# Optimization experiments

Measured on AMD Instinct MI355X. Metric: run time of the kernel, lower is better.

The kernel has to match this reference:

```python
import jax, jax.numpy as jnp
import numpy as np

C = 256
NUM_HEADS = 4
NBLK = 6  # 3 stages x depth 2
WS = (2, 8, 8)   # 3D window
SS = (1, 4, 4)   # shift for odd blocks
N_WIN = WS[0] * WS[1] * WS[2]  # 128 tokens per window
RPB_SIZE = (2 * WS[0] - 1) * (2 * WS[1] - 1) * (2 * WS[2] - 1)  # 675


def _rel_index():
    coords = np.stack(np.meshgrid(np.arange(WS[0]), np.arange(WS[1]), np.arange(WS[2]), indexing='ij'))
    coords = coords.reshape(3, -1)
    rel = (coords[:, :, None] - coords[:, None, :]).transpose(1, 2, 0)
    rel[:, :, 0] += WS[0] - 1
    rel[:, :, 1] += WS[1] - 1
    rel[:, :, 2] += WS[2] - 1
    rel[:, :, 0] *= (2 * WS[1] - 1) * (2 * WS[2] - 1)
    rel[:, :, 1] *= (2 * WS[2] - 1)
    return jnp.asarray(rel.sum(-1))  # [N_WIN, N_WIN]

REL_IDX = _rel_index()


def window_partition(x):
    # [B,D,H,W,C] -> [B*nW, N_WIN, C]
    B, D, H, W, Cc = x.shape
    x = x.reshape(B, D // WS[0], WS[0], H // WS[1], WS[1], W // WS[2], WS[2], Cc)
    return x.transpose(0, 1, 3, 5, 2, 4, 6, 7).reshape(-1, N_WIN, Cc)


def window_reverse(win, B, D, H, W):
    Cc = win.shape[-1]
    x = win.reshape(B, D // WS[0], H // WS[1], W // WS[2], WS[0], WS[1], WS[2], Cc)
    return x.transpose(0, 1, 4, 2, 5, 3, 6, 7).reshape(B, D, H, W, Cc)


def attn_mask(D, H, W):
    # standard shifted-window mask, computed on host constants
    img = np.zeros((1, D, H, W, 1), np.float32)
    cnt = 0
    for d in (slice(0, -WS[0]), slice(-WS[0], -SS[0]), slice(-SS[0], None)):
        for h in (slice(0, -WS[1]), slice(-WS[1], -SS[1]), slice(-SS[1], None)):
            for w in (slice(0, -WS[2]), slice(-WS[2], -SS[2]), slice(-SS[2], None)):
                img[:, d, h, w, :] = cnt
                cnt += 1
    mw = img.reshape(1, D // WS[0], WS[0], H // WS[1], WS[1], W // WS[2], WS[2], 1)
    mw = mw.transpose(0, 1, 3, 5, 2, 4, 6, 7).reshape(-1, N_WIN)
    diff = mw[:, None, :] - mw[:, :, None]
    return jnp.asarray(np.where(diff != 0, -100.0, 0.0).astype(np.float32))  # [nW,N,N]


def layer_norm(x, g, b):
    mu = x.mean(-1, keepdims=True)
    var = ((x - mu) ** 2).mean(-1, keepdims=True)
    return (x - mu) * jax.lax.rsqrt(var + 1e-5) * g + b


def setup_inputs() -> dict:
    key = jax.random.key(0)
    ks = jax.random.split(key, 10)
    f = jax.random.normal
    s = 0.02
    return dict(
        x=f(ks[0], (2, 2, 2, 4096, C), jnp.float32),
        n1w=jnp.ones((NBLK, C), jnp.float32), n1b=jnp.zeros((NBLK, C), jnp.float32),
        qkv_w=f(ks[1], (NBLK, C, 3 * C), jnp.float32) * s, qkv_b=jnp.zeros((NBLK, 3 * C), jnp.float32),
        rpb=f(ks[2], (NBLK, RPB_SIZE, NUM_HEADS), jnp.float32) * s,
        proj_w=f(ks[3], (NBLK, C, C), jnp.float32) * s, proj_b=jnp.zeros((NBLK, C), jnp.float32),
        n2w=jnp.ones((NBLK, C), jnp.float32), n2b=jnp.zeros((NBLK, C), jnp.float32),
        mlp1_w=f(ks[4], (NBLK, C, 4 * C), jnp.float32) * s, mlp1_b=jnp.zeros((NBLK, 4 * C), jnp.float32),
        mlp2_w=f(ks[5], (NBLK, 4 * C, C), jnp.float32) * s, mlp2_b=jnp.zeros((NBLK, C), jnp.float32),
        exp_v_w=f(ks[6], (C, 2 * C), jnp.float32) * s,
        exp_v_nw=jnp.ones((C,), jnp.float32), exp_v_nb=jnp.zeros((C,), jnp.float32),
        exp_t_w=f(ks[7], (C, 2 * C), jnp.float32) * s,
        exp_t_nw=jnp.ones((C,), jnp.float32), exp_t_nb=jnp.zeros((C,), jnp.float32),
    )


def reference(x, n1w, n1b, qkv_w, qkv_b, rpb, proj_w, proj_b, n2w, n2b,
              mlp1_w, mlp1_b, mlp2_w, mlp2_b,
              exp_v_w, exp_v_nw, exp_v_nb, exp_t_w, exp_t_nw, exp_t_nb):
    B, T, V, L, _ = x.shape
    H = W = int(round(np.sqrt(L)))
    NH = NUM_HEADS
    dh = C // NH

    def block(h, i, D, shifted, mask):
        # h: [B, D, L, C]
        sc = h
        y = layer_norm(h, n1w[i], n1b[i]).reshape(B, D, H, W, C)
        if shifted:
            y = jnp.roll(y, (-SS[0], -SS[1], -SS[2]), axis=(1, 2, 3))
        win = window_partition(y)  # [B*nW, N, C]
        qkv = (win @ qkv_w[i] + qkv_b[i]).reshape(-1, N_WIN, 3, NH, dh)
        q, k, v = jnp.moveaxis(qkv, 2, 0)              # [B*nW, N, NH, dh]
        q = q.transpose(0, 2, 1, 3)
        k = k.transpose(0, 2, 1, 3)
        v = v.transpose(0, 2, 1, 3)                     # [B*nW, NH, N, dh]
        attn = jnp.einsum('whqd,whkd->whqk', q, k) * (dh ** -0.5)
        attn = attn + rpb[i][REL_IDX].transpose(2, 0, 1)[None]
        if mask is not None:
            nW = mask.shape[0]
            attn = attn.reshape(B, nW, NH, N_WIN, N_WIN) + mask[None, :, None]
            attn = attn.reshape(-1, NH, N_WIN, N_WIN)
        attn = jax.nn.softmax(attn, axis=-1)
        out = jnp.einsum('whqk,whkd->whqd', attn, v).transpose(0, 2, 1, 3).reshape(-1, N_WIN, C)
        out = out @ proj_w[i] + proj_b[i]
        y = window_reverse(out, B, D, H, W)
        if shifted:
            y = jnp.roll(y, (SS[0], SS[1], SS[2]), axis=(1, 2, 3))
        h = sc + y.reshape(B, D, L, C)
        z = layer_norm(h, n2w[i], n2b[i])
        z = jax.nn.gelu(z @ mlp1_w[i] + mlp1_b[i], approximate=False) @ mlp2_w[i] + mlp2_b[i]
        return h + z

    def stage(h, i0, D):
        mask = attn_mask(D, H, W)
        h = block(h, i0, D, False, None)
        h = block(h, i0 + 1, D, True, mask)
        return h

    # stage 1: swin over D = T*V
    h = x.reshape(B, T * V, L, C)
    h = stage(h, 0, T * V)
    h = h.reshape(B, T, V, L, C)

    # stage 2: view patch expand (V -> 2V) + swin
    h = (h @ exp_v_w).reshape(B, T, V, L, 2, C).transpose(0, 1, 2, 4, 3, 5).reshape(B, T, 2 * V, L, C)
    h = layer_norm(h, exp_v_nw, exp_v_nb)
    V2 = 2 * V
    h = h.reshape(B, T * V2, L, C)
    h = stage(h, 2, T * V2)
    h = h.reshape(B, T, V2, L, C)

    # stage 3: temporal patch expand (T -> 2T) + swin
    h = (h @ exp_t_w).reshape(B, T, V2, L, 2, C).transpose(0, 1, 4, 2, 3, 5).reshape(B, 2 * T, V2, L, C)
    h = layer_norm(h, exp_t_nw, exp_t_nb)
    T2 = 2 * T
    h = h.reshape(B, T2 * V2, L, C)
    h = stage(h, 4, T2 * V2)
    return h.reshape(B, T2, V2, L, C)
```

## Files before the change

kernel.cpp:

```cpp
#include <hip/hip_runtime.h>

typedef __bf16 bf16x8 __attribute__((ext_vector_type(8)));
typedef float f32x4 __attribute__((ext_vector_type(4)));
typedef unsigned short u16;
typedef unsigned int u32;

__device__ __forceinline__ u16 f2b(float f) {
    union { float f; u32 u; } v; v.f = f;
    u32 r = v.u + 0x7fffu + ((v.u >> 16) & 1u);
    return (u16)(r >> 16);
}
__device__ __forceinline__ float b2f(u16 u) {
    union { u32 u; float f; } v; v.u = ((u32)u) << 16; return v.f;
}
__device__ __forceinline__ void gl_lds16(const u16* g, u16* l) {
    __builtin_amdgcn_global_load_lds(
        (const __attribute__((address_space(1))) void*)g,
        (__attribute__((address_space(3))) void*)l, 16, 0, 0);
}

__global__ __launch_bounds__(256) void ln_kernel(
    const float* __restrict__ h, u16* __restrict__ out,
    const float* __restrict__ g, const float* __restrict__ bb,
    int D, int dsh, int shifted, int mode)
{
    const int lane = threadIdx.x & 63;
    const int t = blockIdx.x * 4 + (threadIdx.x >> 6);
    const float4 xv = *(const float4*)(h + (size_t)t * 256 + lane * 4);
    float s = xv.x + xv.y + xv.z + xv.w;
    float s2 = xv.x*xv.x + xv.y*xv.y + xv.z*xv.z + xv.w*xv.w;
    #pragma unroll
    for (int o = 32; o > 0; o >>= 1) { s += __shfl_xor(s, o); s2 += __shfl_xor(s2, o); }
    const float mu = s * 0.00390625f;
    const float var = s2 * 0.00390625f - mu * mu;
    const float rs = 1.0f / sqrtf(var + 1e-5f);
    const int c0 = lane * 4;
    const float4 gv = *(const float4*)(g + c0);
    const float4 bv = *(const float4*)(bb + c0);
    ushort4 o4;
    o4.x = f2b((xv.x - mu) * rs * gv.x + bv.x);
    o4.y = f2b((xv.y - mu) * rs * gv.y + bv.y);
    o4.z = f2b((xv.z - mu) * rs * gv.z + bv.z);
    o4.w = f2b((xv.w - mu) * rs * gv.w + bv.w);
    size_t oidx;
    if (mode == 1) {
        oidx = (size_t)t * 256 + c0;
    } else {
        const int b = t >> (dsh + 12);
        const int rem = t & ((1 << (dsh + 12)) - 1);
        int d = rem >> 12;
        const int l = rem & 4095;
        int hh = l >> 6, ww = l & 63;
        if (shifted) { d = d ? d - 1 : D - 1; hh = (hh - 4) & 63; ww = (ww - 4) & 63; }
        const int widx = (b << (dsh + 5)) + ((d >> 1) << 6) + ((hh >> 3) << 3) + (ww >> 3);
        const int n = ((d & 1) << 6) + ((hh & 7) << 3) + (ww & 7);
        oidx = ((size_t)(widx * 128 + n)) * 256 + c0;
    }
    *(ushort4*)(out + oidx) = o4;
}

__global__ __launch_bounds__(256) void cast_kernel(const float* __restrict__ in, u16* __restrict__ out, int n4)
{
    const int i = blockIdx.x * 256 + threadIdx.x;
    if (i >= n4) return;
    const float4 v = ((const float4*)in)[i];
    ushort4 o; o.x = f2b(v.x); o.y = f2b(v.y); o.z = f2b(v.z); o.w = f2b(v.w);
    ((ushort4*)out)[i] = o;
}

__global__ __launch_bounds__(256) void wt_kernel(const float* __restrict__ src, u16* __restrict__ dst, int K, int N)
{
    const size_t base = (size_t)blockIdx.y * K * N;
    const int idx = blockIdx.x * 256 + threadIdx.x;
    const int k = idx / N, n = idx - k * N;
    dst[base + (size_t)n * K + k] = f2b(src[base + idx]);
}

struct GemmP {
    const u16* A; const u16* Bt;
    int K;
    const float* bias;
    u16* outb;
    float* outf;
    const float* hin; float* hout;
    int D, shifted, nwsh, row_off;
};

template <int EPI>
__global__ __launch_bounds__(256, 2) void gemm_kernel(GemmP p)
{
    __shared__ __align__(16) char smem[33792];
    float* CF = (float*)smem;

    const int tid = threadIdx.x;
    const int m0 = blockIdx.x * 128, n0 = blockIdx.y * 128;
    const int K = p.K;
    const int lane = tid & 63;
    const int wv = tid >> 6;
    const int wm = (wv & 1) * 64, wn = (wv >> 1) * 64;
    const int l16 = lane & 15, quad = lane >> 4;

    f32x4 acc[4][4];
    #pragma unroll
    for (int a = 0; a < 4; a++)
        #pragma unroll
        for (int b = 0; b < 4; b++)
            acc[a][b] = f32x4{0.f, 0.f, 0.f, 0.f};

    const int lrow = lane >> 2;
    const int c16s = (lane & 3) ^ (lrow & 3);
    const int rA0 = wv * 16;
    const u16* Ag = p.A + (size_t)(m0 + rA0 + lrow) * K + c16s * 8;
    const u16* Bg = p.Bt + (size_t)(n0 + rA0 + lrow) * K + c16s * 8;
    const size_t j64 = (size_t)64 * K;
    const int fslot = (quad ^ (l16 & 3)) * 8;

    {
        u16* Al = (u16*)smem + rA0 * 32;
        u16* Bl = (u16*)(smem + 8192) + rA0 * 32;
        gl_lds16(Ag, Al);
        gl_lds16(Ag + j64, Al + 64 * 32);
        gl_lds16(Bg, Bl);
        gl_lds16(Bg + j64, Bl + 64 * 32);
    }
    __syncthreads();

    int kb = 0;
    for (int k0 = 0; k0 < K; k0 += 32, kb ^= 1) {
        if (k0 + 32 < K) {
            char* nb = smem + (kb ^ 1) * 16384;
            u16* Al = (u16*)nb + rA0 * 32;
            u16* Bl = (u16*)(nb + 8192) + rA0 * 32;
            gl_lds16(Ag + k0 + 32, Al);
            gl_lds16(Ag + j64 + k0 + 32, Al + 64 * 32);
            gl_lds16(Bg + k0 + 32, Bl);
            gl_lds16(Bg + j64 + k0 + 32, Bl + 64 * 32);
        }
        const u16* As = (const u16*)(smem + kb * 16384);
        const u16* Bs = (const u16*)(smem + kb * 16384 + 8192);
        bf16x8 af[4], bfr[4];
        #pragma unroll
        for (int mt = 0; mt < 4; mt++) af[mt] = *(const bf16x8*)(As + (wm + mt * 16 + l16) * 32 + fslot);
        #pragma unroll
        for (int nt = 0; nt < 4; nt++) bfr[nt] = *(const bf16x8*)(Bs + (wn + nt * 16 + l16) * 32 + fslot);
        #pragma unroll
        for (int mt = 0; mt < 4; mt++)
            #pragma unroll
            for (int nt = 0; nt < 4; nt++)
                acc[mt][nt] = __builtin_amdgcn_mfma_f32_16x16x32_bf16(af[mt], bfr[nt], acc[mt][nt], 0, 0, 0);
        __syncthreads();
    }

    const int crow = tid >> 2;
    const int p4 = (tid & 3) * 4;
    #pragma unroll
    for (int c = 0; c < 2; c++) {
        if (c) __syncthreads();
        if ((wv & 1) == c) {
            #pragma unroll
            for (int mt = 0; mt < 4; mt++)
                #pragma unroll
                for (int nt = 0; nt < 4; nt++)
                    #pragma unroll
                    for (int i = 0; i < 4; i++)
                        CF[(mt * 16 + quad * 4 + i) * 132 + wn + nt * 16 + l16] = acc[mt][nt][i];
        }
        __syncthreads();
        const int rowg = m0 + c * 64 + crow;
        size_t tokbase = 0;
        if constexpr (EPI == 1) {
            const int widx = rowg >> 7, n = rowg & 127;
            const int b = widx >> p.nwsh, rem = widx & ((1 << p.nwsh) - 1);
            int dd = ((rem >> 6) << 1) + (n >> 6);
            int hh = (((rem >> 3) & 7) << 3) + ((n >> 3) & 7);
            int ww = ((rem & 7) << 3) + (n & 7);
            if (p.shifted) { dd = (dd + 1 == p.D) ? 0 : dd + 1; hh = (hh + 4) & 63; ww = (ww + 4) & 63; }
            tokbase = ((size_t)((b * p.D + dd) * 4096 + hh * 64 + ww)) * 256;
        } else if constexpr (EPI == 3) {
            tokbase = (size_t)(p.row_off + rowg) * 256;
        }
        #pragma unroll
        for (int j = 0; j < 8; j++) {
            const int colf = j * 16 + p4;
            const int colg = n0 + colf;
            const float4 t = *(const float4*)(CF + crow * 132 + colf);
            const float4 bi = (EPI <= 3) ? *(const float4*)(p.bias + colg) : float4{0.f,0.f,0.f,0.f};
            if constexpr (EPI == 0) {
                const float sc = (colg < 256) ? 0.125f : 1.0f;
                ushort4 pk;
                pk.x = f2b((t.x + bi.x) * sc);
                pk.y = f2b((t.y + bi.y) * sc);
                pk.z = f2b((t.z + bi.z) * sc);
                pk.w = f2b((t.w + bi.w) * sc);
                *(ushort4*)(p.outb + (size_t)rowg * 768 + colg) = pk;
            } else if constexpr (EPI == 1 || EPI == 3) {
                const float* hi = p.hin + tokbase + colg;
                float* ho = p.hout + tokbase + colg;
                const float4 r = *(const float4*)hi;
                float4 o;
                o.x = r.x + t.x + bi.x;
                o.y = r.y + t.y + bi.y;
                o.z = r.z + t.z + bi.z;
                o.w = r.w + t.w + bi.w;
                *(float4*)ho = o;
            } else if constexpr (EPI == 2) {
                float4 g4;
                g4.x = t.x + bi.x; g4.y = t.y + bi.y; g4.z = t.z + bi.z; g4.w = t.w + bi.w;
                ushort4 pk;
                pk.x = f2b(0.5f * g4.x * (1.0f + erff(g4.x * 0.7071067811865475f)));
                pk.y = f2b(0.5f * g4.y * (1.0f + erff(g4.y * 0.7071067811865475f)));
                pk.z = f2b(0.5f * g4.z * (1.0f + erff(g4.z * 0.7071067811865475f)));
                pk.w = f2b(0.5f * g4.w * (1.0f + erff(g4.w * 0.7071067811865475f)));
                *(ushort4*)(p.outb + (size_t)rowg * 1024 + colg) = pk;
            } else {
                *(float4*)(p.outf + (size_t)rowg * 512 + colg) = t;
            }
        }
    }
}

struct MlpP {
    const u16* A;
    const u16* W1t;
    const u16* W2t;
    const float* b1;
    const float* b2;
    const float* hin;
    float* hout;
};

__global__ __launch_bounds__(512, 1) void mlp_fused_kernel(MlpP p)
{
    __shared__ __align__(16) char smem[149504];
    u16* S = (u16*)(smem + 131072);
    float* CF = (float*)smem;

    const int tid = threadIdx.x;
    const int lane = tid & 63;
    const int wv = tid >> 6;
    const int l16 = lane & 15, quad = lane >> 4;
    const int tok0 = blockIdx.x * 128;

    const int wm = (wv & 3) * 32;
    const int wn1 = (wv >> 2) * 32;
    const int wn2 = (wv >> 2) * 128;
    const int fslot = (quad ^ (l16 & 3)) * 8;

    const int srow = lane >> 2;
    const int sslotg = (lane & 3) ^ (srow & 3);
    const int w1row = (wv & 3) * 16 + srow;

    bf16x8 afr[2][8];
    #pragma unroll
    for (int mt = 0; mt < 2; mt++)
        #pragma unroll
        for (int kt = 0; kt < 8; kt++)
            afr[mt][kt] = *(const bf16x8*)(p.A + (size_t)(tok0 + wm + mt * 16 + l16) * 256 + kt * 32 + quad * 8);

    f32x4 acc2[2][8];
    #pragma unroll
    for (int mt = 0; mt < 2; mt++)
        #pragma unroll
        for (int nt = 0; nt < 8; nt++)
            acc2[mt][nt] = f32x4{0.f, 0.f, 0.f, 0.f};

    float b2v[8];
    #pragma unroll
    for (int nt = 0; nt < 8; nt++) b2v[nt] = p.b2[wn2 + nt * 16 + l16];

    auto stage = [&](int c) {
        char* w1b = smem + (c & 1) * 32768;
        char* w2b = smem + 65536 + (c & 1) * 32768;
        #pragma unroll
        for (int pp = 0; pp < 4; pp++) {
            const int panel = pp * 2 + (wv >> 2);
            gl_lds16(p.W1t + (size_t)(c * 64 + w1row) * 256 + panel * 32 + sslotg * 8,
                     (u16*)(w1b + pp * 8192 + wv * 1024));
        }
        #pragma unroll
        for (int pp = 0; pp < 4; pp++) {
            const int row = (pp & 1) * 128 + wv * 16 + srow;
            const int panel = pp >> 1;
            gl_lds16(p.W2t + (size_t)row * 1024 + c * 64 + panel * 32 + sslotg * 8,
                     (u16*)(w2b + pp * 8192 + wv * 1024));
        }
    };

    stage(0);
    __syncthreads();

    for (int c = 0; c < 16; c++) {
        if (c + 1 < 16) stage(c + 1);

        const u16* W1c = (const u16*)(smem + (c & 1) * 32768);
        f32x4 acc1[2][2];
        #pragma unroll
        for (int mt = 0; mt < 2; mt++)
            #pragma unroll
            for (int nt = 0; nt < 2; nt++)
                acc1[mt][nt] = f32x4{0.f, 0.f, 0.f, 0.f};
        #pragma unroll
        for (int kt = 0; kt < 8; kt++) {
            bf16x8 bw[2];
            #pragma unroll
            for (int nt = 0; nt < 2; nt++)
                bw[nt] = *(const bf16x8*)(W1c + kt * 2048 + (wn1 + nt * 16 + l16) * 32 + fslot);
            #pragma unroll
            for (int mt = 0; mt < 2; mt++)
                #pragma unroll
                for (int nt = 0; nt < 2; nt++)
                    acc1[mt][nt] = __builtin_amdgcn_mfma_f32_16x16x32_bf16(afr[mt][kt], bw[nt], acc1[mt][nt], 0, 0, 0);
        }

        #pragma unroll
        for (int nt = 0; nt < 2; nt++) {
            const float b1v = p.b1[c * 64 + wn1 + nt * 16 + l16];
            #pragma unroll
            for (int mt = 0; mt < 2; mt++)
                #pragma unroll
                for (int i = 0; i < 4; i++) {
                    const float x = acc1[mt][nt][i] + b1v;
                    const float g = 0.5f * x * (1.0f + erff(x * 0.7071067811865475f));
                    S[(wm + mt * 16 + quad * 4 + i) * 72 + wn1 + nt * 16 + l16] = f2b(g);
                }
        }
        __syncthreads();

        const u16* W2c = (const u16*)(smem + 65536 + (c & 1) * 32768);
        #pragma unroll
        for (int kt = 0; kt < 2; kt++) {
            bf16x8 ap[2], bw[8];
            #pragma unroll
            for (int mt = 0; mt < 2; mt++)
                ap[mt] = *(const bf16x8*)(S + (wm + mt * 16 + l16) * 72 + kt * 32 + quad * 8);
            #pragma unroll
            for (int nt = 0; nt < 8; nt++)
                bw[nt] = *(const bf16x8*)(W2c + kt * 8192 + (wn2 + nt * 16 + l16) * 32 + fslot);
            #pragma unroll
            for (int mt = 0; mt < 2; mt++)
                #pragma unroll
                for (int nt = 0; nt < 8; nt++)
                    acc2[mt][nt] = __builtin_amdgcn_mfma_f32_16x16x32_bf16(ap[mt], bw[nt], acc2[mt][nt], 0, 0, 0);
        }
        __syncthreads();
    }

    #pragma unroll
    for (int cc = 0; cc < 2; cc++) {
        __syncthreads();
        if (((wv & 3) >> 1) == cc) {
            const int rb = wm & 63;
            #pragma unroll
            for (int mt = 0; mt < 2; mt++)
                #pragma unroll
                for (int nt = 0; nt < 8; nt++)
                    #pragma unroll
                    for (int i = 0; i < 4; i++)
                        CF[(rb + mt * 16 + quad * 4 + i) * 260 + wn2 + nt * 16 + l16] = acc2[mt][nt][i] + b2v[nt];
        }
        __syncthreads();
        #pragma unroll
        for (int jj = 0; jj < 8; jj++) {
            const int idx = jj * 512 + tid;
            const int row = idx >> 6, c4 = (idx & 63) << 2;
            const size_t g = (size_t)(tok0 + cc * 64 + row) * 256 + c4;
            const float4 t = *(const float4*)(CF + row * 260 + c4);
            const float4 r = *(const float4*)(p.hin + g);
            float4 o;
            o.x = t.x + r.x; o.y = t.y + r.y; o.z = t.z + r.z; o.w = t.w + r.w;
            *(float4*)(p.hout + g) = o;
        }
    }
}

__global__ __launch_bounds__(256, 2) void attn_mfma_kernel(
    const u16* __restrict__ qkv, u16* __restrict__ att,
    const float* __restrict__ rpbp, int D, int shifted, int w0g, int nwsh)
{
    __shared__ __align__(16) char smem[57856];
    u16* Qs = (u16*)smem;
    u16* Ks = (u16*)(smem + 18432);
    u16* Ps = (u16*)smem;
    u16* Vt = (u16*)(smem + 36864);
    float* rb = (float*)(smem + 54272);
    int* lbl = (int*)(smem + 56972);

    const int wloc = blockIdx.x;
    const int head = blockIdx.y;
    const int tid = threadIdx.x;
    const u16* base = qkv + (size_t)wloc * 98304;

    #pragma unroll
    for (int it = 0; it < 4; it++) {
        const int id = it * 256 + tid;
        const int row = id >> 3, oct = id & 7;
        const size_t ro = (size_t)row * 768 + head * 64 + oct * 8;
        *(uint4*)(Qs + row * 72 + oct * 8) = *(const uint4*)(base + ro);
        *(uint4*)(Ks + row * 72 + oct * 8) = *(const uint4*)(base + ro + 256);
        uint4 vv = *(const uint4*)(base + ro + 512);
        const u16* vp = (const u16*)&vv;
        #pragma unroll
        for (int q = 0; q < 8; q++) Vt[(oct * 8 + q) * 136 + row] = vp[q];
    }
    for (int j = tid; j < 675; j += 256) rb[j] = rpbp[j * 4 + head];
    if (tid < 128) {
        int lv = 0;
        if (shifted) {
            const int widx = w0g + wloc;
            const int rem = widx & ((1 << nwsh) - 1);
            const int d0 = rem >> 6, h0 = (rem >> 3) & 7, w0 = rem & 7;
            const int wd = tid >> 6, wh = (tid >> 3) & 7, ww = tid & 7;
            const int rd = (d0 < (D >> 1) - 1) ? 0 : (1 + wd);
            const int rh = (h0 < 7) ? 0 : (1 + (wh >= 4));
            const int rw = (w0 < 7) ? 0 : (1 + (ww >= 4));
            lv = rd * 9 + rh * 3 + rw;
        }
        lbl[tid] = lv;
    }
    __syncthreads();

    const int wq = tid >> 6;
    const int lane = tid & 63;
    const int l16 = lane & 15, quad = lane >> 4;
    const int myrow0 = wq * 32;

    f32x4 sc[2][8];
    #pragma unroll
    for (int mt = 0; mt < 2; mt++)
        #pragma unroll
        for (int nt = 0; nt < 8; nt++)
            sc[mt][nt] = f32x4{0.f, 0.f, 0.f, 0.f};
    #pragma unroll
    for (int kt = 0; kt < 2; kt++) {
        bf16x8 aq[2];
        #pragma unroll
        for (int mt = 0; mt < 2; mt++)
            aq[mt] = *(const bf16x8*)(Qs + (myrow0 + mt * 16 + l16) * 72 + kt * 32 + quad * 8);
        bf16x8 bk[8];
        #pragma unroll
        for (int nt = 0; nt < 8; nt++)
            bk[nt] = *(const bf16x8*)(Ks + (nt * 16 + l16) * 72 + kt * 32 + quad * 8);
        #pragma unroll
        for (int mt = 0; mt < 2; mt++)
            #pragma unroll
            for (int nt = 0; nt < 8; nt++)
                sc[mt][nt] = __builtin_amdgcn_mfma_f32_16x16x32_bf16(aq[mt], bk[nt], sc[mt][nt], 0, 0, 0);
    }

    float linv[2][4];
    #pragma unroll
    for (int mt = 0; mt < 2; mt++) {
        #pragma unroll
        for (int i = 0; i < 4; i++) {
            const int row = myrow0 + mt * 16 + quad * 4 + i;
            const int rbase = ((row >> 6) + 1) * 225 + (((row >> 3) & 7) + 7) * 15 + ((row & 7) + 7);
            const int lq = lbl[row];
            float mx = -1e30f;
            float sv[8];
            #pragma unroll
            for (int nt = 0; nt < 8; nt++) {
                const int col = nt * 16 + l16;
                float v = sc[mt][nt][i] + rb[rbase - (col >> 6) * 225 - ((col >> 3) & 7) * 15 - (col & 7)];
                if (shifted && lq != lbl[col]) v -= 100.0f;
                sv[nt] = v;
                mx = fmaxf(mx, v);
            }
            #pragma unroll
            for (int o = 1; o < 16; o <<= 1) mx = fmaxf(mx, __shfl_xor(mx, o));
            float l = 0.0f;
            #pragma unroll
            for (int nt = 0; nt < 8; nt++) {
                const float pp = __expf(sv[nt] - mx);
                sc[mt][nt][i] = pp;
                l += pp;
            }
            #pragma unroll
            for (int o = 1; o < 16; o <<= 1) l += __shfl_xor(l, o);
            linv[mt][i] = 1.0f / l;
        }
    }

    __syncthreads();
    #pragma unroll
    for (int mt = 0; mt < 2; mt++)
        #pragma unroll
        for (int nt = 0; nt < 8; nt++)
            #pragma unroll
            for (int i = 0; i < 4; i++)
                Ps[(myrow0 + mt * 16 + quad * 4 + i) * 136 + nt * 16 + l16] = f2b(sc[mt][nt][i]);

    f32x4 oc[2][4];
    #pragma unroll
    for (int mt = 0; mt < 2; mt++)
        #pragma unroll
        for (int nt = 0; nt < 4; nt++)
            oc[mt][nt] = f32x4{0.f, 0.f, 0.f, 0.f};
    #pragma unroll
    for (int kt = 0; kt < 4; kt++) {
        bf16x8 ap[2];
        #pragma unroll
        for (int mt = 0; mt < 2; mt++)
            ap[mt] = *(const bf16x8*)(Ps + (myrow0 + mt * 16 + l16) * 136 + kt * 32 + quad * 8);
        bf16x8 bv[4];
        #pragma unroll
        for (int nt = 0; nt < 4; nt++)
            bv[nt] = *(const bf16x8*)(Vt + (nt * 16 + l16) * 136 + kt * 32 + quad * 8);
        #pragma unroll
        for (int mt = 0; mt < 2; mt++)
            #pragma unroll
            for (int nt = 0; nt < 4; nt++)
                oc[mt][nt] = __builtin_amdgcn_mfma_f32_16x16x32_bf16(ap[mt], bv[nt], oc[mt][nt], 0, 0, 0);
    }

    #pragma unroll
    for (int mt = 0; mt < 2; mt++)
        #pragma unroll
        for (int nt = 0; nt < 4; nt++)
            #pragma unroll
            for (int i = 0; i < 4; i++) {
                const int row = myrow0 + mt * 16 + quad * 4 + i;
                const int col = nt * 16 + l16;
                att[(size_t)(wloc * 128 + row) * 256 + head * 64 + col] = f2b(oc[mt][nt][i] * linv[mt][i]);
            }
}

__global__ __launch_bounds__(256) void expand_ln_kernel(
    const float* __restrict__ sc, float* __restrict__ hout,
    const float* __restrict__ g, const float* __restrict__ bb,
    int it0, int typ)
{
    const int lane = threadIdx.x & 63;
    const int ot = blockIdx.x * 4 + (threadIdx.x >> 6);
    const int itl = ot >> 1, e = ot & 1;
    const float4 xv = *(const float4*)(sc + (size_t)itl * 512 + e * 256 + lane * 4);
    float s = xv.x + xv.y + xv.z + xv.w;
    float s2 = xv.x*xv.x + xv.y*xv.y + xv.z*xv.z + xv.w*xv.w;
    #pragma unroll
    for (int o = 32; o > 0; o >>= 1) { s += __shfl_xor(s, o); s2 += __shfl_xor(s2, o); }
    const float mu = s * 0.00390625f;
    const float var = s2 * 0.00390625f - mu * mu;
    const float rs = 1.0f / sqrtf(var + 1e-5f);
    const int c0 = lane * 4;
    const float4 gv = *(const float4*)(g + c0);
    const float4 bv = *(const float4*)(bb + c0);
    float4 y;
    y.x = (xv.x - mu) * rs * gv.x + bv.x;
    y.y = (xv.y - mu) * rs * gv.y + bv.y;
    y.z = (xv.z - mu) * rs * gv.z + bv.z;
    y.w = (xv.w - mu) * rs * gv.w + bv.w;
    const int it = it0 + itl;
    size_t otg;
    if (typ == 0) {
        const int b = it >> 14, rr = it & 16383;
        const int t = rr >> 13, v = (rr >> 12) & 1, l = rr & 4095;
        otg = (size_t)(((b * 2 + t) * 4 + v * 2 + e) * 4096 + l);
    } else {
        const int b = it >> 15, rr = it & 32767;
        const int t = rr >> 14, v2 = (rr >> 12) & 3, l = rr & 4095;
        otg = (size_t)(((b * 4 + t * 2 + e) * 4 + v2) * 4096 + l);
    }
    *(float4*)(hout + otg * 256 + c0) = y;
}

extern "C" void kernel_launch(void* const* d_in, const int* in_sizes, int n_in,
                              void* d_out, int out_size, void* d_ws, size_t ws_size,
                              hipStream_t stream)
{
    const float* x      = (const float*)d_in[0];
    const float* n1w    = (const float*)d_in[1];
    const float* n1b    = (const float*)d_in[2];
    const float* qkv_w  = (const float*)d_in[3];
    const float* qkv_b  = (const float*)d_in[4];
    const float* rpb    = (const float*)d_in[5];
    const float* proj_w = (const float*)d_in[6];
    const float* proj_b = (const float*)d_in[7];
    const float* n2w    = (const float*)d_in[8];
    const float* n2b    = (const float*)d_in[9];
    const float* mlp1_w = (const float*)d_in[10];
    const float* mlp1_b = (const float*)d_in[11];
    const float* mlp2_w = (const float*)d_in[12];
    const float* mlp2_b = (const float*)d_in[13];
    const float* expv_w = (const float*)d_in[14];
    const float* expv_nw= (const float*)d_in[15];
    const float* expv_nb= (const float*)d_in[16];
    const float* expt_w = (const float*)d_in[17];
    const float* expt_nw= (const float*)d_in[18];
    const float* expt_nb= (const float*)d_in[19];
    (void)in_sizes; (void)n_in; (void)out_size;

    if (ws_size < 352321536ULL) return;

    char* ws = (char*)d_ws;
    float* h    = (float*)ws;
    u16*  winb  = (u16*)(ws + 134217728LL);
    u16*  att   = (u16*)(ws + 134217728LL + 67108864LL);
    char* scr   = ws + 134217728LL + 2LL * 67108864LL;
    u16*  scrb  = (u16*)scr;
    float* scrf = (float*)scr;
    u16* qkvT   = (u16*)(ws + 134217728LL + 3LL * 67108864LL);
    u16* projT  = qkvT + 6 * 768 * 256;
    u16* mlp1T  = projT + 6 * 256 * 256;
    u16* mlp2T  = mlp1T + 6 * 1024 * 256;
    u16* expvT  = mlp2T + 6 * 256 * 1024;
    u16* exptT  = expvT + 512 * 256;

    wt_kernel<<<dim3(768, 6), 256, 0, stream>>>(qkv_w, qkvT, 256, 768);
    wt_kernel<<<dim3(256, 6), 256, 0, stream>>>(proj_w, projT, 256, 256);
    wt_kernel<<<dim3(1024, 6), 256, 0, stream>>>(mlp1_w, mlp1T, 256, 1024);
    wt_kernel<<<dim3(1024, 6), 256, 0, stream>>>(mlp2_w, mlp2T, 1024, 256);
    wt_kernel<<<dim3(512, 1), 256, 0, stream>>>(expv_w, expvT, 256, 512);
    wt_kernel<<<dim3(512, 1), 256, 0, stream>>>(expt_w, exptT, 256, 512);
    hipMemcpyAsync(h, x, 33554432ULL, hipMemcpyDeviceToDevice, stream);

    for (int s = 0; s < 3; s++) {
        const int D = 4 << s;
        const int dsh = 2 + s;
        const int nwsh = dsh + 5;
        const int tokens = 2 * D * 4096;
        const int nch = tokens / 32768;
        for (int j = 0; j < 2; j++) {
            const int i = 2 * s + j;
            ln_kernel<<<dim3(tokens / 4), 256, 0, stream>>>(h, winb, n1w + i * 256, n1b + i * 256, D, dsh, j, 0);
            for (int c = 0; c < nch; c++) {
                GemmP gq{};
                gq.A = winb + (size_t)c * 32768 * 256;
                gq.Bt = qkvT + (size_t)i * 768 * 256;
                gq.K = 256; gq.bias = qkv_b + i * 768; gq.outb = scrb;
                gemm_kernel<0><<<dim3(256, 6), 256, 0, stream>>>(gq);
                attn_mfma_kernel<<<dim3(256, 4), 256, 0, stream>>>(scrb, att + (size_t)c * 32768 * 256,
                                                                   rpb + i * 675 * 4, D, j, c * 256, nwsh);
            }
            GemmP gp{};
            gp.A = att; gp.Bt = projT + (size_t)i * 256 * 256; gp.K = 256;
            gp.bias = proj_b + i * 256; gp.hin = h; gp.hout = h;
            gp.D = D; gp.shifted = j; gp.nwsh = nwsh;
            gemm_kernel<1><<<dim3(tokens / 128, 2), 256, 0, stream>>>(gp);
            ln_kernel<<<dim3(tokens / 4), 256, 0, stream>>>(h, winb, n2w + i * 256, n2b + i * 256, D, dsh, 0, 1);
            MlpP mp{};
            mp.A = winb;
            mp.W1t = mlp1T + (size_t)i * 1024 * 256;
            mp.W2t = mlp2T + (size_t)i * 256 * 1024;
            mp.b1 = mlp1_b + i * 1024;
            mp.b2 = mlp2_b + i * 256;
            mp.hin = h;
            mp.hout = (s == 2 && j == 1) ? (float*)d_out : h;
            mlp_fused_kernel<<<dim3(tokens / 128), 512, 0, stream>>>(mp);
        }
        if (s < 2) {
            const int ntok = tokens;
            cast_kernel<<<dim3(ntok * 64 / 256), 256, 0, stream>>>(h, winb, ntok * 64);
            const u16* eT = (s == 0) ? expvT : exptT;
            const float* eg = (s == 0) ? expv_nw : expt_nw;
            const float* eb = (s == 0) ? expv_nb : expt_nb;
            for (int c = 0; c < ntok / 32768; c++) {
                GemmP ge{};
                ge.A = winb + (size_t)c * 32768 * 256; ge.Bt = eT; ge.K = 256; ge.outf = scrf;
                gemm_kernel<4><<<dim3(256, 4), 256, 0, stream>>>(ge);
                expand_ln_kernel<<<dim3(16384), 256, 0, stream>>>(scrf, h, eg, eb, c * 32768, s);
            }
        }
    }
}
```

Baseline: 2.568 ms.

## Keep MLP hidden activations in registers via transposed GEMM1 and permuted W2

The fused MLP kernel now computes GEMM1 as W1^T·A so that each wave's output fragment already has the layout of the A operand for GEMM2. This removes the LDS staging buffer for GELU outputs and one barrier per chunk, and each wave now owns 16 tokens across all 256 output columns. To make this work, the mlp2 weight transpose permutes its K index to match the register fragment order. Exact erf GELU is replaced by a tanh-form approximation built from exp and rcp, which changes numerics slightly, and the larger per-wave accumulator set raises register pressure.

```diff
diff --git a/kernel.cpp b/kernel.cpp
--- a/kernel.cpp
+++ b/kernel.cpp
@@ -74,6 +74,18 @@
     const int idx = blockIdx.x * 256 + threadIdx.x;
     const int k = idx / N, n = idx - k * N;
     dst[base + (size_t)n * K + k] = f2b(src[base + idx]);
+}
+
+__global__ __launch_bounds__(256) void wt2_kernel(const float* __restrict__ src, u16* __restrict__ dst)
+{
+    const size_t base = (size_t)blockIdx.y * 1024 * 256;
+    const int kp = blockIdx.x;
+    const int n = threadIdx.x;
+    const int kl = kp & 63;
+    const int kt = kl >> 5, q = (kl >> 3) & 3, e = kl & 7;
+    const int m = (2 * kt + (e >> 2)) * 16 + q * 4 + (e & 3);
+    const int kn = (kp & ~63) + m;
+    dst[base + (size_t)n * 1024 + kp] = f2b(src[base + (size_t)kn * 256 + n]);
 }
 
 struct GemmP {
@@ -231,8 +243,7 @@
 
 __global__ __launch_bounds__(512, 1) void mlp_fused_kernel(MlpP p)
 {
-    __shared__ __align__(16) char smem[149504];
-    u16* S = (u16*)(smem + 131072);
+    __shared__ __align__(16) char smem[131072];
     float* CF = (float*)smem;
 
     const int tid = threadIdx.x;
@@ -240,33 +251,25 @@
     const int wv = tid >> 6;
     const int l16 = lane & 15, quad = lane >> 4;
     const int tok0 = blockIdx.x * 128;
-
-    const int wm = (wv & 3) * 32;
-    const int wn1 = (wv >> 2) * 32;
-    const int wn2 = (wv >> 2) * 128;
+    const int wtok = wv * 16;
     const int fslot = (quad ^ (l16 & 3)) * 8;
 
     const int srow = lane >> 2;
     const int sslotg = (lane & 3) ^ (srow & 3);
     const int w1row = (wv & 3) * 16 + srow;
 
-    bf16x8 afr[2][8];
-    #pragma unroll
-    for (int mt = 0; mt < 2; mt++)
-        #pragma unroll
-        for (int kt = 0; kt < 8; kt++)
-            afr[mt][kt] = *(const bf16x8*)(p.A + (size_t)(tok0 + wm + mt * 16 + l16) * 256 + kt * 32 + quad * 8);
-
-    f32x4 acc2[2][8];
-    #pragma unroll
-    for (int mt = 0; mt < 2; mt++)
-        #pragma unroll
-        for (int nt = 0; nt < 8; nt++)
-            acc2[mt][nt] = f32x4{0.f, 0.f, 0.f, 0.f};
-
-    float b2v[8];
-    #pragma unroll
-    for (int nt = 0; nt < 8; nt++) b2v[nt] = p.b2[wn2 + nt * 16 + l16];
+    bf16x8 afr[8];
+    #pragma unroll
+    for (int kt = 0; kt < 8; kt++)
+        afr[kt] = *(const bf16x8*)(p.A + (size_t)(tok0 + wtok + l16) * 256 + kt * 32 + quad * 8);
+
+    f32x4 acc2[16];
+    #pragma unroll
+    for (int nt = 0; nt < 16; nt++) acc2[nt] = f32x4{0.f, 0.f, 0.f, 0.f};
+
+    float b2v[16];
+    #pragma unroll
+    for (int nt = 0; nt < 16; nt++) b2v[nt] = p.b2[nt * 16 + l16];
 
     auto stage = [&](int c) {
         char* w1b = smem + (c & 1) * 32768;
@@ -289,58 +292,55 @@
     stage(0);
     __syncthreads();
 
+    #pragma unroll 2
     for (int c = 0; c < 16; c++) {
         if (c + 1 < 16) stage(c + 1);
 
+        float b1v[4][4];
+        #pragma unroll
+        for (int n = 0; n < 4; n++)
+            #pragma unroll
+            for (int i = 0; i < 4; i++)
+                b1v[n][i] = p.b1[c * 64 + n * 16 + quad * 4 + i];
+
         const u16* W1c = (const u16*)(smem + (c & 1) * 32768);
-        f32x4 acc1[2][2];
-        #pragma unroll
-        for (int mt = 0; mt < 2; mt++)
-            #pragma unroll
-            for (int nt = 0; nt < 2; nt++)
-                acc1[mt][nt] = f32x4{0.f, 0.f, 0.f, 0.f};
+        f32x4 acc1[4];
+        #pragma unroll
+        for (int n = 0; n < 4; n++) acc1[n] = f32x4{0.f, 0.f, 0.f, 0.f};
         #pragma unroll
         for (int kt = 0; kt < 8; kt++) {
-            bf16x8 bw[2];
-            #pragma unroll
-            for (int nt = 0; nt < 2; nt++)
-                bw[nt] = *(const bf16x8*)(W1c + kt * 2048 + (wn1 + nt * 16 + l16) * 32 + fslot);
-            #pragma unroll
-            for (int mt = 0; mt < 2; mt++)
-                #pragma unroll
-                for (int nt = 0; nt < 2; nt++)
-                    acc1[mt][nt] = __builtin_amdgcn_mfma_f32_16x16x32_bf16(afr[mt][kt], bw[nt], acc1[mt][nt], 0, 0, 0);
-        }
-
-        #pragma unroll
-        for (int nt = 0; nt < 2; nt++) {
-            const float b1v = p.b1[c * 64 + wn1 + nt * 16 + l16];
-            #pragma unroll
-            for (int mt = 0; mt < 2; mt++)
-                #pragma unroll
-                for (int i = 0; i < 4; i++) {
-                    const float x = acc1[mt][nt][i] + b1v;
-                    const float g = 0.5f * x * (1.0f + erff(x * 0.7071067811865475f));
-                    S[(wm + mt * 16 + quad * 4 + i) * 72 + wn1 + nt * 16 + l16] = f2b(g);
-                }
-        }
-        __syncthreads();
+            bf16x8 w1f[4];
+            #pragma unroll
+            for (int n = 0; n < 4; n++)
+                w1f[n] = *(const bf16x8*)(W1c + kt * 2048 + (n * 16 + l16) * 32 + fslot);
+            #pragma unroll
+            for (int n = 0; n < 4; n++)
+                acc1[n] = __builtin_amdgcn_mfma_f32_16x16x32_bf16(w1f[n], afr[kt], acc1[n], 0, 0, 0);
+        }
+
+        bf16x8 pa0, pa1;
+        #pragma unroll
+        for (int n = 0; n < 4; n++) {
+            #pragma unroll
+            for (int i = 0; i < 4; i++) {
+                const float x = acc1[n][i] + b1v[n][i];
+                const float u = x * (1.0f + 0.044715f * x * x);
+                const float em = __expf(-1.5957691216f * u);
+                const float g = x * __builtin_amdgcn_rcpf(1.0f + em);
+                if (n < 2) pa0[(n & 1) * 4 + i] = (__bf16)g;
+                else       pa1[(n & 1) * 4 + i] = (__bf16)g;
+            }
+        }
 
         const u16* W2c = (const u16*)(smem + 65536 + (c & 1) * 32768);
         #pragma unroll
         for (int kt = 0; kt < 2; kt++) {
-            bf16x8 ap[2], bw[8];
-            #pragma unroll
-            for (int mt = 0; mt < 2; mt++)
-                ap[mt] = *(const bf16x8*)(S + (wm + mt * 16 + l16) * 72 + kt * 32 + quad * 8);
-            #pragma unroll
-            for (int nt = 0; nt < 8; nt++)
-                bw[nt] = *(const bf16x8*)(W2c + kt * 8192 + (wn2 + nt * 16 + l16) * 32 + fslot);
-            #pragma unroll
-            for (int mt = 0; mt < 2; mt++)
-                #pragma unroll
-                for (int nt = 0; nt < 8; nt++)
-                    acc2[mt][nt] = __builtin_amdgcn_mfma_f32_16x16x32_bf16(ap[mt], bw[nt], acc2[mt][nt], 0, 0, 0);
+            const bf16x8 pk = kt ? pa1 : pa0;
+            #pragma unroll
+            for (int nt = 0; nt < 16; nt++) {
+                const bf16x8 w2f = *(const bf16x8*)(W2c + kt * 8192 + (nt * 16 + l16) * 32 + fslot);
+                acc2[nt] = __builtin_amdgcn_mfma_f32_16x16x32_bf16(pk, w2f, acc2[nt], 0, 0, 0);
+            }
         }
         __syncthreads();
     }
@@ -348,15 +348,13 @@
     #pragma unroll
     for (int cc = 0; cc < 2; cc++) {
         __syncthreads();
-        if (((wv & 3) >> 1) == cc) {
-            const int rb = wm & 63;
-            #pragma unroll
-            for (int mt = 0; mt < 2; mt++)
+        if ((wv >> 2) == cc) {
+            const int rb = (wv & 3) * 16;
+            #pragma unroll
+            for (int nt = 0; nt < 16; nt++)
                 #pragma unroll
-                for (int nt = 0; nt < 8; nt++)
-                    #pragma unroll
-                    for (int i = 0; i < 4; i++)
-                        CF[(rb + mt * 16 + quad * 4 + i) * 260 + wn2 + nt * 16 + l16] = acc2[mt][nt][i] + b2v[nt];
+                for (int i = 0; i < 4; i++)
+                    CF[(rb + quad * 4 + i) * 260 + nt * 16 + l16] = acc2[nt][i] + b2v[nt];
         }
         __syncthreads();
         #pragma unroll
@@ -607,7 +605,7 @@
     wt_kernel<<<dim3(768, 6), 256, 0, stream>>>(qkv_w, qkvT, 256, 768);
     wt_kernel<<<dim3(256, 6), 256, 0, stream>>>(proj_w, projT, 256, 256);
     wt_kernel<<<dim3(1024, 6), 256, 0, stream>>>(mlp1_w, mlp1T, 256, 1024);
-    wt_kernel<<<dim3(1024, 6), 256, 0, stream>>>(mlp2_w, mlp2T, 1024, 256);
+    wt2_kernel<<<dim3(1024, 6), 256, 0, stream>>>(mlp2_w, mlp2T);
     wt_kernel<<<dim3(512, 1), 256, 0, stream>>>(expv_w, expvT, 256, 512);
     wt_kernel<<<dim3(512, 1), 256, 0, stream>>>(expt_w, exptT, 256, 512);
     hipMemcpyAsync(h, x, 33554432ULL, hipMemcpyDeviceToDevice, stream);
```

New measurement: 2.557 ms. About the same (-0.4%).
